# Performance work log

Measured on AMD Instinct MI355X. Metric: run time of the kernel, lower is better.

## Reference

```python
import jax, jax.numpy as jnp
import numpy as np

B, S, E, Q, A = 32, 2048, 1024, 1024, 512

def setup_inputs() -> dict:
    key = jax.random.key(0)
    k1, k2, k3, k4, k5 = jax.random.split(key, 5)
    scale = lambda d: 1.0 / np.sqrt(d)
    return {
        "inputs": jax.random.normal(k1, (B, S, E), dtype=jnp.float32),
        "query": jax.random.normal(k2, (B, Q), dtype=jnp.float32),
        "W_in": jax.random.normal(k3, (E, A), dtype=jnp.float32) * scale(E),
        "W_q": jax.random.normal(k4, (Q, A), dtype=jnp.float32) * scale(Q),
        "w_att": jax.random.normal(k5, (A,), dtype=jnp.float32) * scale(A),
    }

def reference(inputs, query, W_in, W_q, w_att):
    # projected inputs: [B, S, A]
    proj_in = jnp.einsum("bse,ea->bsa", inputs, W_in)
    # projected query, broadcast over S: [B, 1, A]
    proj_q = (query @ W_q)[:, None, :]
    # additive scores: [B, S]
    scores = jnp.einsum("bsa,a->bs", jnp.tanh(proj_in + proj_q), w_att)
    weights = jax.nn.softmax(scores, axis=1)  # over sequence dim
    # context over PROJECTED inputs (as in original): [B, A]
    context = jnp.einsum("bs,bsa->ba", weights, proj_in)
    return context
```

## Files before the change

### kernel.cpp

```cpp
#include <hip/hip_runtime.h>
#include <hip/hip_fp16.h>
#include <cstdint>
#include <cstddef>

#define Bb 32
#define Ss 2048
#define Ee 1024
#define Qq 1024
#define Aa 512

typedef _Float16 half8 __attribute__((ext_vector_type(8)));
typedef _Float16 half4 __attribute__((ext_vector_type(4)));
typedef float f32x4 __attribute__((ext_vector_type(4)));

#define WS_PROJQ 0u
#define WS_MPART 65536u
#define WS_LPART 69632u
#define WS_CTXP  73728u
#define WS_WWS   2170880u

__device__ __forceinline__ float fast_tanh(float x) {
  float e = __expf(2.0f * x);
  return 1.0f - __fdividef(2.0f, e + 1.0f);
}

__global__ void k_convw(const float* __restrict__ win, _Float16* __restrict__ wws) {
  int gid = blockIdx.x * 256 + threadIdx.x;
  int a  = gid & 511;
  int ks = (gid >> 9) & 3;
  int kt = gid >> 11;
  int k0 = kt * 32 + ks * 8;
  half8 v;
  #pragma unroll
  for (int j = 0; j < 8; ++j) v[j] = (_Float16)win[(size_t)(k0 + j) * Aa + a];
  *(half8*)(wws + ((size_t)kt * 16384 + (size_t)ks * 4096 + (size_t)a * 8)) = v;
}

__global__ void k_projq(const float* __restrict__ query, const float* __restrict__ wq,
                        float* __restrict__ projq) {
  __shared__ float red[256];
  int b  = blockIdx.y;
  int al = threadIdx.x & 63;
  int eq = threadIdx.x >> 6;
  int a  = blockIdx.x * 64 + al;
  const float* q = query + (size_t)b * Qq;
  float s = 0.f;
  int e0 = eq * 256;
  #pragma unroll 4
  for (int e = e0; e < e0 + 256; ++e)
    s += q[e] * wq[(size_t)e * Aa + a];
  red[threadIdx.x] = s;
  __syncthreads();
  if (eq == 0)
    projq[(size_t)b * Aa + a] = red[al] + red[al + 64] + red[al + 128] + red[al + 192];
}

__global__ __launch_bounds__(512, 4)
void k_main(const float* __restrict__ inp, const _Float16* __restrict__ wws,
            const float* __restrict__ projq, const float* __restrict__ watt,
            float* __restrict__ mpart, float* __restrict__ lpart,
            float* __restrict__ ctxp)
{
  __shared__ __align__(16) char pool[73728];
  _Float16* AldsB = (_Float16*)pool;
  _Float16* BldsB = (_Float16*)(pool + 8192);

  const int tid = threadIdx.x;
  const int l   = tid & 63;
  const int w   = tid >> 6;
  const int lr  = l & 15;
  const int kb  = l >> 4;
  const int wr  = w >> 2;
  const int wc  = w & 3;
  const int b   = blockIdx.y;
  const int ch  = blockIdx.x;

  const int arow = tid >> 3;
  const int kq   = tid & 7;
  const float* asrc = inp + ((size_t)(b * Ss + ch * 64 + arow)) * Ee + kq * 4;
  const int awoff = ((kq >> 1) * 64 + arow) * 8 + (kq & 1) * 4;

  const char* bsrc0 = (const char*)wws + (size_t)tid * 16;

  f32x4 acc[2][8];
  #pragma unroll
  for (int m = 0; m < 2; ++m)
    #pragma unroll
    for (int n = 0; n < 8; ++n) acc[m][n] = (f32x4){0.f, 0.f, 0.f, 0.f};

  {
    float4 x = *(const float4*)(asrc);
    half4 h; h[0]=(_Float16)x.x; h[1]=(_Float16)x.y; h[2]=(_Float16)x.z; h[3]=(_Float16)x.w;
    *(half4*)(AldsB + awoff) = h;
    #pragma unroll
    for (int i = 0; i < 4; ++i)
      __builtin_amdgcn_global_load_lds(
        (const __attribute__((address_space(1))) void*)(bsrc0 + i * 8192),
        (__attribute__((address_space(3))) void*)(pool + 8192 + tid * 16 + i * 8192),
        16, 0, 0);
  }
  float4 areg = *(const float4*)(asrc + 32);
  __syncthreads();

  int p = 0;
  for (int kt = 0; kt < 32; ++kt) {
    if (kt < 31) {
      half4 h; h[0]=(_Float16)areg.x; h[1]=(_Float16)areg.y; h[2]=(_Float16)areg.z; h[3]=(_Float16)areg.w;
      *(half4*)(AldsB + (p ^ 1) * 2048 + awoff) = h;
      const char* bs = bsrc0 + (size_t)(kt + 1) * 32768;
      #pragma unroll
      for (int i = 0; i < 4; ++i)
        __builtin_amdgcn_global_load_lds(
          (const __attribute__((address_space(1))) void*)(bs + i * 8192),
          (__attribute__((address_space(3))) void*)(pool + 8192 + (p ^ 1) * 32768 + tid * 16 + i * 8192),
          16, 0, 0);
    }
    __builtin_amdgcn_sched_barrier(0);
    const int ktn2 = (kt < 30) ? kt + 2 : 31;
    float4 anext = *(const float4*)(asrc + (size_t)ktn2 * 32);
    __builtin_amdgcn_sched_barrier(0);

    const _Float16* Ap = AldsB + p * 2048;
    half8 af0 = *(const half8*)(Ap + (kb * 64 + wr * 32 +      lr) * 8);
    half8 af1 = *(const half8*)(Ap + (kb * 64 + wr * 32 + 16 + lr) * 8);
    const _Float16* Bp = BldsB + p * 16384 + (kb * 512 + wc * 128 + lr) * 8;
    half8 bf0 = *(const half8*)(Bp);
    half8 bf1 = *(const half8*)(Bp + 16 * 8);
    half8 bf2 = *(const half8*)(Bp + 32 * 8);
    half8 bf3 = *(const half8*)(Bp + 48 * 8);

    acc[0][0] = __builtin_amdgcn_mfma_f32_16x16x32_f16(af0, bf0, acc[0][0], 0, 0, 0);
    acc[1][0] = __builtin_amdgcn_mfma_f32_16x16x32_f16(af1, bf0, acc[1][0], 0, 0, 0);
    acc[0][1] = __builtin_amdgcn_mfma_f32_16x16x32_f16(af0, bf1, acc[0][1], 0, 0, 0);
    acc[1][1] = __builtin_amdgcn_mfma_f32_16x16x32_f16(af1, bf1, acc[1][1], 0, 0, 0);
    acc[0][2] = __builtin_amdgcn_mfma_f32_16x16x32_f16(af0, bf2, acc[0][2], 0, 0, 0);
    acc[1][2] = __builtin_amdgcn_mfma_f32_16x16x32_f16(af1, bf2, acc[1][2], 0, 0, 0);
    acc[0][3] = __builtin_amdgcn_mfma_f32_16x16x32_f16(af0, bf3, acc[0][3], 0, 0, 0);
    acc[1][3] = __builtin_amdgcn_mfma_f32_16x16x32_f16(af1, bf3, acc[1][3], 0, 0, 0);

    half8 bf4 = *(const half8*)(Bp + 64 * 8);
    half8 bf5 = *(const half8*)(Bp + 80 * 8);
    half8 bf6 = *(const half8*)(Bp + 96 * 8);
    half8 bf7 = *(const half8*)(Bp + 112 * 8);
    acc[0][4] = __builtin_amdgcn_mfma_f32_16x16x32_f16(af0, bf4, acc[0][4], 0, 0, 0);
    acc[1][4] = __builtin_amdgcn_mfma_f32_16x16x32_f16(af1, bf4, acc[1][4], 0, 0, 0);
    acc[0][5] = __builtin_amdgcn_mfma_f32_16x16x32_f16(af0, bf5, acc[0][5], 0, 0, 0);
    acc[1][5] = __builtin_amdgcn_mfma_f32_16x16x32_f16(af1, bf5, acc[1][5], 0, 0, 0);
    acc[0][6] = __builtin_amdgcn_mfma_f32_16x16x32_f16(af0, bf6, acc[0][6], 0, 0, 0);
    acc[1][6] = __builtin_amdgcn_mfma_f32_16x16x32_f16(af1, bf6, acc[1][6], 0, 0, 0);
    acc[0][7] = __builtin_amdgcn_mfma_f32_16x16x32_f16(af0, bf7, acc[0][7], 0, 0, 0);
    acc[1][7] = __builtin_amdgcn_mfma_f32_16x16x32_f16(af1, bf7, acc[1][7], 0, 0, 0);

    __builtin_amdgcn_sched_barrier(0);
    asm volatile("s_waitcnt vmcnt(1)" ::: "memory");
    asm volatile("s_waitcnt lgkmcnt(0)" ::: "memory");
    __builtin_amdgcn_sched_barrier(0);
    __builtin_amdgcn_s_barrier();
    __builtin_amdgcn_sched_barrier(0);

    p ^= 1;
    areg = anext;
  }

  __syncthreads();
  float* pq_s = (float*)pool;
  float* wa_s = (float*)(pool + 2048);
  float (*sc4)[4] = (float(*)[4])(pool + 4096);
  float* pbuf = (float*)(pool + 5120);
  float (*ctx2)[512] = (float(*)[512])(pool + 8192);

  pq_s[tid] = projq[(size_t)b * Aa + tid];
  wa_s[tid] = watt[tid];
  __syncthreads();

  float sp[2][4];
  #pragma unroll
  for (int m = 0; m < 2; ++m)
    #pragma unroll
    for (int j = 0; j < 4; ++j) sp[m][j] = 0.f;

  #pragma unroll
  for (int n = 0; n < 8; ++n) {
    int col = wc * 128 + n * 16 + lr;
    float wan = wa_s[col], pqn = pq_s[col];
    #pragma unroll
    for (int m = 0; m < 2; ++m)
      #pragma unroll
      for (int j = 0; j < 4; ++j)
        sp[m][j] += fast_tanh(acc[m][n][j] + pqn) * wan;
  }
  #pragma unroll
  for (int m = 0; m < 2; ++m)
    #pragma unroll
    for (int j = 0; j < 4; ++j) {
      float v = sp[m][j];
      v += __shfl_xor(v, 1);
      v += __shfl_xor(v, 2);
      v += __shfl_xor(v, 4);
      v += __shfl_xor(v, 8);
      sp[m][j] = v;
    }
  if (lr == 0) {
    #pragma unroll
    for (int m = 0; m < 2; ++m)
      #pragma unroll
      for (int j = 0; j < 4; ++j)
        sc4[wr * 32 + m * 16 + kb * 4 + j][wc] = sp[m][j];
  }
  __syncthreads();

  const int pi = b * 32 + ch;
  if (tid < 64) {
    float s = sc4[tid][0] + sc4[tid][1] + sc4[tid][2] + sc4[tid][3];
    float mx = s;
    #pragma unroll
    for (int off = 1; off < 64; off <<= 1) mx = fmaxf(mx, __shfl_xor(mx, off));
    float pe = __expf(s - mx);
    float ls = pe;
    #pragma unroll
    for (int off = 1; off < 64; off <<= 1) ls += __shfl_xor(ls, off);
    pbuf[tid] = pe;
    if (tid == 0) { mpart[pi] = mx; lpart[pi] = ls; }
  }
  __syncthreads();

  float cv[8];
  #pragma unroll
  for (int n = 0; n < 8; ++n) cv[n] = 0.f;
  #pragma unroll
  for (int m = 0; m < 2; ++m)
    #pragma unroll
    for (int j = 0; j < 4; ++j) {
      float pw = pbuf[wr * 32 + m * 16 + kb * 4 + j];
      #pragma unroll
      for (int n = 0; n < 8; ++n) cv[n] += pw * acc[m][n][j];
    }
  #pragma unroll
  for (int n = 0; n < 8; ++n) {
    float v = cv[n];
    v += __shfl_xor(v, 16);
    v += __shfl_xor(v, 32);
    cv[n] = v;
  }
  if (l < 16) {
    #pragma unroll
    for (int n = 0; n < 8; ++n) ctx2[wr][wc * 128 + n * 16 + l] = cv[n];
  }
  __syncthreads();

  ctxp[(size_t)pi * 512 + tid] = ctx2[0][tid] + ctx2[1][tid];
}

__global__ void k_comb(const float* __restrict__ mpart, const float* __restrict__ lpart,
                       const float* __restrict__ ctxp, float* __restrict__ out) {
  int b = blockIdx.x, a = threadIdx.x;
  float Mg = -1e30f;
  #pragma unroll 8
  for (int i = 0; i < 32; ++i) Mg = fmaxf(Mg, mpart[b * 32 + i]);
  float den = 0.f, s = 0.f;
  #pragma unroll 8
  for (int i = 0; i < 32; ++i) {
    float e = __expf(mpart[b * 32 + i] - Mg);
    den += lpart[b * 32 + i] * e;
    s   += ctxp[((size_t)(b * 32 + i)) * 512 + a] * e;
  }
  out[(size_t)b * 512 + a] = s / den;
}

extern "C" void kernel_launch(void* const* d_in, const int* in_sizes, int n_in,
                              void* d_out, int out_size, void* d_ws, size_t ws_size,
                              hipStream_t stream) {
  const float* inputs = (const float*)d_in[0];
  const float* query  = (const float*)d_in[1];
  const float* W_in   = (const float*)d_in[2];
  const float* W_q    = (const float*)d_in[3];
  const float* w_att  = (const float*)d_in[4];
  float* out = (float*)d_out;

  char* ws = (char*)d_ws;
  float*    projq = (float*)(ws + WS_PROJQ);
  float*    mpart = (float*)(ws + WS_MPART);
  float*    lpart = (float*)(ws + WS_LPART);
  float*    ctxp  = (float*)(ws + WS_CTXP);
  _Float16* wws   = (_Float16*)(ws + WS_WWS);

  k_convw<<<256, 256, 0, stream>>>(W_in, wws);
  k_projq<<<dim3(8, 32), 256, 0, stream>>>(query, W_q, projq);
  k_main<<<dim3(32, 32), 512, 0, stream>>>(inputs, wws, projq, w_att, mpart, lpart, ctxp);
  k_comb<<<32, 512, 0, stream>>>(mpart, lpart, ctxp, out);
}
```

Baseline: 145.4 us.

## Restructure main GEMM to 64-wide K tiles with per-wave column ownership

The main fused kernel now processes K in 16 steps of 64 instead of 32 steps of 32, so it needs half as many block barriers. Each wave owns a 64-column slice across all 64 rows (a 4x4 MFMA tile), where before the waves were split 2x4 over rows and columns. The A tile is loaded as 8 halves per thread, MFMA groups are wrapped in s_setprio, and the final context is written straight to global without an LDS reduction. LDS per block doubles to 144KB and the occupancy hint drops to 2, which may limit how much latency other blocks can hide.

```diff
diff --git a/kernel.cpp b/kernel.cpp
--- a/kernel.cpp
+++ b/kernel.cpp
@@ -10,7 +10,6 @@
 #define Aa 512
 
 typedef _Float16 half8 __attribute__((ext_vector_type(8)));
-typedef _Float16 half4 __attribute__((ext_vector_type(4)));
 typedef float f32x4 __attribute__((ext_vector_type(4)));
 
 #define WS_PROJQ 0u
@@ -23,6 +22,8 @@
   float e = __expf(2.0f * x);
   return 1.0f - __fdividef(2.0f, e + 1.0f);
 }
+
+#define MFMA16(d, a8, b8) d = __builtin_amdgcn_mfma_f32_16x16x32_f16(a8, b8, d, 0, 0, 0)
 
 __global__ void k_convw(const float* __restrict__ win, _Float16* __restrict__ wws) {
   int gid = blockIdx.x * 256 + threadIdx.x;
@@ -55,142 +56,164 @@
     projq[(size_t)b * Aa + a] = red[al] + red[al + 64] + red[al + 128] + red[al + 192];
 }
 
-__global__ __launch_bounds__(512, 4)
+__global__ __launch_bounds__(512, 2)
 void k_main(const float* __restrict__ inp, const _Float16* __restrict__ wws,
             const float* __restrict__ projq, const float* __restrict__ watt,
             float* __restrict__ mpart, float* __restrict__ lpart,
             float* __restrict__ ctxp)
 {
-  __shared__ __align__(16) char pool[73728];
+  __shared__ __align__(16) char pool[147456];
   _Float16* AldsB = (_Float16*)pool;
-  _Float16* BldsB = (_Float16*)(pool + 8192);
+  _Float16* BldsB = (_Float16*)(pool + 16384);
 
   const int tid = threadIdx.x;
   const int l   = tid & 63;
   const int w   = tid >> 6;
   const int lr  = l & 15;
   const int kb  = l >> 4;
-  const int wr  = w >> 2;
-  const int wc  = w & 3;
   const int b   = blockIdx.y;
   const int ch  = blockIdx.x;
 
   const int arow = tid >> 3;
-  const int kq   = tid & 7;
-  const float* asrc = inp + ((size_t)(b * Ss + ch * 64 + arow)) * Ee + kq * 4;
-  const int awoff = ((kq >> 1) * 64 + arow) * 8 + (kq & 1) * 4;
+  const int akq  = tid & 7;
+  const float* asrc = inp + ((size_t)(b * Ss + ch * 64 + arow)) * Ee + akq * 8;
+  const int awoff = (akq * 64 + arow) * 8;
 
   const char* bsrc0 = (const char*)wws + (size_t)tid * 16;
 
-  f32x4 acc[2][8];
-  #pragma unroll
-  for (int m = 0; m < 2; ++m)
-    #pragma unroll
-    for (int n = 0; n < 8; ++n) acc[m][n] = (f32x4){0.f, 0.f, 0.f, 0.f};
+  f32x4 acc[4][4];
+  #pragma unroll
+  for (int m = 0; m < 4; ++m)
+    #pragma unroll
+    for (int n = 0; n < 4; ++n) acc[m][n] = (f32x4){0.f, 0.f, 0.f, 0.f};
 
   {
-    float4 x = *(const float4*)(asrc);
-    half4 h; h[0]=(_Float16)x.x; h[1]=(_Float16)x.y; h[2]=(_Float16)x.z; h[3]=(_Float16)x.w;
-    *(half4*)(AldsB + awoff) = h;
-    #pragma unroll
-    for (int i = 0; i < 4; ++i)
+    #pragma unroll
+    for (int i = 0; i < 8; ++i)
       __builtin_amdgcn_global_load_lds(
         (const __attribute__((address_space(1))) void*)(bsrc0 + i * 8192),
-        (__attribute__((address_space(3))) void*)(pool + 8192 + tid * 16 + i * 8192),
+        (__attribute__((address_space(3))) void*)(pool + 16384 + tid * 16 + i * 8192),
         16, 0, 0);
-  }
-  float4 areg = *(const float4*)(asrc + 32);
-  __syncthreads();
-
-  int p = 0;
-  for (int kt = 0; kt < 32; ++kt) {
-    if (kt < 31) {
-      half4 h; h[0]=(_Float16)areg.x; h[1]=(_Float16)areg.y; h[2]=(_Float16)areg.z; h[3]=(_Float16)areg.w;
-      *(half4*)(AldsB + (p ^ 1) * 2048 + awoff) = h;
-      const char* bs = bsrc0 + (size_t)(kt + 1) * 32768;
+    float4 x0 = *(const float4*)(asrc);
+    float4 x1 = *(const float4*)(asrc + 4);
+    half8 h;
+    h[0]=(_Float16)x0.x; h[1]=(_Float16)x0.y; h[2]=(_Float16)x0.z; h[3]=(_Float16)x0.w;
+    h[4]=(_Float16)x1.x; h[5]=(_Float16)x1.y; h[6]=(_Float16)x1.z; h[7]=(_Float16)x1.w;
+    *(half8*)(AldsB + awoff) = h;
+  }
+  __syncthreads();
+
+  int pp = 0;
+  for (int t = 0; t < 16; ++t) {
+    const _Float16* Abase = AldsB + pp * 4096;
+    const _Float16* Bbase = BldsB + pp * 32768;
+
+    half8 bf0 = *(const half8*)(Bbase + (kb * 512 + w * 64      + lr) * 8);
+    half8 bf1 = *(const half8*)(Bbase + (kb * 512 + w * 64 + 16 + lr) * 8);
+    half8 bf2 = *(const half8*)(Bbase + (kb * 512 + w * 64 + 32 + lr) * 8);
+    half8 bf3 = *(const half8*)(Bbase + (kb * 512 + w * 64 + 48 + lr) * 8);
+    half8 af0 = *(const half8*)(Abase + (kb * 64      + lr) * 8);
+    half8 af1 = *(const half8*)(Abase + (kb * 64 + 16 + lr) * 8);
+
+    float4 aL0, aL1;
+    if (t < 15) {
+      const char* bs = bsrc0 + (size_t)(t + 1) * 65536;
       #pragma unroll
-      for (int i = 0; i < 4; ++i)
+      for (int i = 0; i < 8; ++i)
         __builtin_amdgcn_global_load_lds(
           (const __attribute__((address_space(1))) void*)(bs + i * 8192),
-          (__attribute__((address_space(3))) void*)(pool + 8192 + (p ^ 1) * 32768 + tid * 16 + i * 8192),
+          (__attribute__((address_space(3))) void*)(pool + 16384 + (pp ^ 1) * 65536 + tid * 16 + i * 8192),
           16, 0, 0);
-    }
-    __builtin_amdgcn_sched_barrier(0);
-    const int ktn2 = (kt < 30) ? kt + 2 : 31;
-    float4 anext = *(const float4*)(asrc + (size_t)ktn2 * 32);
-    __builtin_amdgcn_sched_barrier(0);
-
-    const _Float16* Ap = AldsB + p * 2048;
-    half8 af0 = *(const half8*)(Ap + (kb * 64 + wr * 32 +      lr) * 8);
-    half8 af1 = *(const half8*)(Ap + (kb * 64 + wr * 32 + 16 + lr) * 8);
-    const _Float16* Bp = BldsB + p * 16384 + (kb * 512 + wc * 128 + lr) * 8;
-    half8 bf0 = *(const half8*)(Bp);
-    half8 bf1 = *(const half8*)(Bp + 16 * 8);
-    half8 bf2 = *(const half8*)(Bp + 32 * 8);
-    half8 bf3 = *(const half8*)(Bp + 48 * 8);
-
-    acc[0][0] = __builtin_amdgcn_mfma_f32_16x16x32_f16(af0, bf0, acc[0][0], 0, 0, 0);
-    acc[1][0] = __builtin_amdgcn_mfma_f32_16x16x32_f16(af1, bf0, acc[1][0], 0, 0, 0);
-    acc[0][1] = __builtin_amdgcn_mfma_f32_16x16x32_f16(af0, bf1, acc[0][1], 0, 0, 0);
-    acc[1][1] = __builtin_amdgcn_mfma_f32_16x16x32_f16(af1, bf1, acc[1][1], 0, 0, 0);
-    acc[0][2] = __builtin_amdgcn_mfma_f32_16x16x32_f16(af0, bf2, acc[0][2], 0, 0, 0);
-    acc[1][2] = __builtin_amdgcn_mfma_f32_16x16x32_f16(af1, bf2, acc[1][2], 0, 0, 0);
-    acc[0][3] = __builtin_amdgcn_mfma_f32_16x16x32_f16(af0, bf3, acc[0][3], 0, 0, 0);
-    acc[1][3] = __builtin_amdgcn_mfma_f32_16x16x32_f16(af1, bf3, acc[1][3], 0, 0, 0);
-
-    half8 bf4 = *(const half8*)(Bp + 64 * 8);
-    half8 bf5 = *(const half8*)(Bp + 80 * 8);
-    half8 bf6 = *(const half8*)(Bp + 96 * 8);
-    half8 bf7 = *(const half8*)(Bp + 112 * 8);
-    acc[0][4] = __builtin_amdgcn_mfma_f32_16x16x32_f16(af0, bf4, acc[0][4], 0, 0, 0);
-    acc[1][4] = __builtin_amdgcn_mfma_f32_16x16x32_f16(af1, bf4, acc[1][4], 0, 0, 0);
-    acc[0][5] = __builtin_amdgcn_mfma_f32_16x16x32_f16(af0, bf5, acc[0][5], 0, 0, 0);
-    acc[1][5] = __builtin_amdgcn_mfma_f32_16x16x32_f16(af1, bf5, acc[1][5], 0, 0, 0);
-    acc[0][6] = __builtin_amdgcn_mfma_f32_16x16x32_f16(af0, bf6, acc[0][6], 0, 0, 0);
-    acc[1][6] = __builtin_amdgcn_mfma_f32_16x16x32_f16(af1, bf6, acc[1][6], 0, 0, 0);
-    acc[0][7] = __builtin_amdgcn_mfma_f32_16x16x32_f16(af0, bf7, acc[0][7], 0, 0, 0);
-    acc[1][7] = __builtin_amdgcn_mfma_f32_16x16x32_f16(af1, bf7, acc[1][7], 0, 0, 0);
-
-    __builtin_amdgcn_sched_barrier(0);
-    asm volatile("s_waitcnt vmcnt(1)" ::: "memory");
-    asm volatile("s_waitcnt lgkmcnt(0)" ::: "memory");
-    __builtin_amdgcn_sched_barrier(0);
-    __builtin_amdgcn_s_barrier();
-    __builtin_amdgcn_sched_barrier(0);
-
-    p ^= 1;
-    areg = anext;
+      __builtin_amdgcn_sched_barrier(0);
+      const float* ap = asrc + (size_t)(t + 1) * 64;
+      aL0 = *(const float4*)(ap);
+      aL1 = *(const float4*)(ap + 4);
+      __builtin_amdgcn_sched_barrier(0);
+    }
+
+    __builtin_amdgcn_s_setprio(1);
+    MFMA16(acc[0][0], af0, bf0); MFMA16(acc[0][1], af0, bf1);
+    MFMA16(acc[0][2], af0, bf2); MFMA16(acc[0][3], af0, bf3);
+    MFMA16(acc[1][0], af1, bf0); MFMA16(acc[1][1], af1, bf1);
+    MFMA16(acc[1][2], af1, bf2); MFMA16(acc[1][3], af1, bf3);
+    __builtin_amdgcn_s_setprio(0);
+
+    half8 af2 = *(const half8*)(Abase + (kb * 64 + 32 + lr) * 8);
+    half8 af3 = *(const half8*)(Abase + (kb * 64 + 48 + lr) * 8);
+    __builtin_amdgcn_s_setprio(1);
+    MFMA16(acc[2][0], af2, bf0); MFMA16(acc[2][1], af2, bf1);
+    MFMA16(acc[2][2], af2, bf2); MFMA16(acc[2][3], af2, bf3);
+    MFMA16(acc[3][0], af3, bf0); MFMA16(acc[3][1], af3, bf1);
+    MFMA16(acc[3][2], af3, bf2); MFMA16(acc[3][3], af3, bf3);
+    __builtin_amdgcn_s_setprio(0);
+
+    bf0 = *(const half8*)(Bbase + ((4 + kb) * 512 + w * 64      + lr) * 8);
+    bf1 = *(const half8*)(Bbase + ((4 + kb) * 512 + w * 64 + 16 + lr) * 8);
+    bf2 = *(const half8*)(Bbase + ((4 + kb) * 512 + w * 64 + 32 + lr) * 8);
+    bf3 = *(const half8*)(Bbase + ((4 + kb) * 512 + w * 64 + 48 + lr) * 8);
+    af0 = *(const half8*)(Abase + ((4 + kb) * 64      + lr) * 8);
+    af1 = *(const half8*)(Abase + ((4 + kb) * 64 + 16 + lr) * 8);
+    __builtin_amdgcn_s_setprio(1);
+    MFMA16(acc[0][0], af0, bf0); MFMA16(acc[0][1], af0, bf1);
+    MFMA16(acc[0][2], af0, bf2); MFMA16(acc[0][3], af0, bf3);
+    MFMA16(acc[1][0], af1, bf0); MFMA16(acc[1][1], af1, bf1);
+    MFMA16(acc[1][2], af1, bf2); MFMA16(acc[1][3], af1, bf3);
+    __builtin_amdgcn_s_setprio(0);
+
+    af2 = *(const half8*)(Abase + ((4 + kb) * 64 + 32 + lr) * 8);
+    af3 = *(const half8*)(Abase + ((4 + kb) * 64 + 48 + lr) * 8);
+    if (t < 15) {
+      __builtin_amdgcn_sched_barrier(0);
+      half8 h;
+      h[0]=(_Float16)aL0.x; h[1]=(_Float16)aL0.y; h[2]=(_Float16)aL0.z; h[3]=(_Float16)aL0.w;
+      h[4]=(_Float16)aL1.x; h[5]=(_Float16)aL1.y; h[6]=(_Float16)aL1.z; h[7]=(_Float16)aL1.w;
+      *(half8*)(AldsB + (pp ^ 1) * 4096 + awoff) = h;
+      __builtin_amdgcn_sched_barrier(0);
+    }
+    __builtin_amdgcn_s_setprio(1);
+    MFMA16(acc[2][0], af2, bf0); MFMA16(acc[2][1], af2, bf1);
+    MFMA16(acc[2][2], af2, bf2); MFMA16(acc[2][3], af2, bf3);
+    MFMA16(acc[3][0], af3, bf0); MFMA16(acc[3][1], af3, bf1);
+    MFMA16(acc[3][2], af3, bf2); MFMA16(acc[3][3], af3, bf3);
+    __builtin_amdgcn_s_setprio(0);
+
+    if (t < 15) {
+      asm volatile("s_waitcnt lgkmcnt(0)" ::: "memory");
+      __builtin_amdgcn_sched_barrier(0);
+      __builtin_amdgcn_s_barrier();
+      __builtin_amdgcn_sched_barrier(0);
+    }
+    pp ^= 1;
   }
 
   __syncthreads();
   float* pq_s = (float*)pool;
   float* wa_s = (float*)(pool + 2048);
-  float (*sc4)[4] = (float(*)[4])(pool + 4096);
-  float* pbuf = (float*)(pool + 5120);
-  float (*ctx2)[512] = (float(*)[512])(pool + 8192);
+  float (*sc8)[8] = (float(*)[8])(pool + 4096);
+  float* pbuf = (float*)(pool + 6144);
 
   pq_s[tid] = projq[(size_t)b * Aa + tid];
   wa_s[tid] = watt[tid];
   __syncthreads();
 
-  float sp[2][4];
-  #pragma unroll
-  for (int m = 0; m < 2; ++m)
+  float sp[4][4];
+  #pragma unroll
+  for (int m = 0; m < 4; ++m)
     #pragma unroll
     for (int j = 0; j < 4; ++j) sp[m][j] = 0.f;
 
   #pragma unroll
-  for (int n = 0; n < 8; ++n) {
-    int col = wc * 128 + n * 16 + lr;
+  for (int n = 0; n < 4; ++n) {
+    int col = w * 64 + n * 16 + lr;
     float wan = wa_s[col], pqn = pq_s[col];
     #pragma unroll
-    for (int m = 0; m < 2; ++m)
+    for (int m = 0; m < 4; ++m)
       #pragma unroll
       for (int j = 0; j < 4; ++j)
         sp[m][j] += fast_tanh(acc[m][n][j] + pqn) * wan;
   }
   #pragma unroll
-  for (int m = 0; m < 2; ++m)
+  for (int m = 0; m < 4; ++m)
     #pragma unroll
     for (int j = 0; j < 4; ++j) {
       float v = sp[m][j];
@@ -202,16 +225,18 @@
     }
   if (lr == 0) {
     #pragma unroll
-    for (int m = 0; m < 2; ++m)
+    for (int m = 0; m < 4; ++m)
       #pragma unroll
       for (int j = 0; j < 4; ++j)
-        sc4[wr * 32 + m * 16 + kb * 4 + j][wc] = sp[m][j];
+        sc8[m * 16 + kb * 4 + j][w] = sp[m][j];
   }
   __syncthreads();
 
   const int pi = b * 32 + ch;
   if (tid < 64) {
-    float s = sc4[tid][0] + sc4[tid][1] + sc4[tid][2] + sc4[tid][3];
+    float s = 0.f;
+    #pragma unroll
+    for (int q = 0; q < 8; ++q) s += sc8[tid][q];
     float mx = s;
     #pragma unroll
     for (int off = 1; off < 64; off <<= 1) mx = fmaxf(mx, __shfl_xor(mx, off));
@@ -224,19 +249,19 @@
   }
   __syncthreads();
 
-  float cv[8];
-  #pragma unroll
-  for (int n = 0; n < 8; ++n) cv[n] = 0.f;
-  #pragma unroll
-  for (int m = 0; m < 2; ++m)
+  float cv[4];
+  #pragma unroll
+  for (int n = 0; n < 4; ++n) cv[n] = 0.f;
+  #pragma unroll
+  for (int m = 0; m < 4; ++m)
     #pragma unroll
     for (int j = 0; j < 4; ++j) {
-      float pw = pbuf[wr * 32 + m * 16 + kb * 4 + j];
+      float pw = pbuf[m * 16 + kb * 4 + j];
       #pragma unroll
-      for (int n = 0; n < 8; ++n) cv[n] += pw * acc[m][n][j];
-    }
-  #pragma unroll
-  for (int n = 0; n < 8; ++n) {
+      for (int n = 0; n < 4; ++n) cv[n] += pw * acc[m][n][j];
+    }
+  #pragma unroll
+  for (int n = 0; n < 4; ++n) {
     float v = cv[n];
     v += __shfl_xor(v, 16);
     v += __shfl_xor(v, 32);
@@ -244,11 +269,9 @@
   }
   if (l < 16) {
     #pragma unroll
-    for (int n = 0; n < 8; ++n) ctx2[wr][wc * 128 + n * 16 + l] = cv[n];
-  }
-  __syncthreads();
-
-  ctxp[(size_t)pi * 512 + tid] = ctx2[0][tid] + ctx2[1][tid];
+    for (int n = 0; n < 4; ++n)
+      ctxp[(size_t)pi * 512 + w * 64 + n * 16 + l] = cv[n];
+  }
 }
 
 __global__ void k_comb(const float* __restrict__ mpart, const float* __restrict__ lpart,
```

Result: slower. 175.8 us (+20.9%).

## Switch main GEMM to 32x32x16 MFMA with 1x8 wave tiling

Applied to the files above, without the earlier changes.

The projection GEMM moves from 16x16x32 MFMA tiles on a 2x4 wave grid to 32x32x16 MFMA tiles, with each wave owning all 64 rows and a 64-column slice. The aim is fewer LDS fragment reads per MFMA and larger, more efficient matrix instructions. The score and context epilogues are rewritten for the 32x32 accumulator layout, so the context is written straight from registers without an LDS reduction stage. The hand-placed waitcnt and sched barriers are replaced by a plain __syncthreads, with the A-tile LDS store moved after the MFMAs. That barrier may now also wait on the outstanding prefetch load, which could add stalls in the main loop.

```diff
diff --git a/kernel.cpp b/kernel.cpp
--- a/kernel.cpp
+++ b/kernel.cpp
@@ -11,7 +11,7 @@
 
 typedef _Float16 half8 __attribute__((ext_vector_type(8)));
 typedef _Float16 half4 __attribute__((ext_vector_type(4)));
-typedef float f32x4 __attribute__((ext_vector_type(4)));
+typedef float f32x16 __attribute__((ext_vector_type(16)));
 
 #define WS_PROJQ 0u
 #define WS_MPART 65536u
@@ -23,6 +23,8 @@
   float e = __expf(2.0f * x);
   return 1.0f - __fdividef(2.0f, e + 1.0f);
 }
+
+#define MFMA32(d, a8, b8) d = __builtin_amdgcn_mfma_f32_32x32x16_f16(a8, b8, d, 0, 0, 0)
 
 __global__ void k_convw(const float* __restrict__ win, _Float16* __restrict__ wws) {
   int gid = blockIdx.x * 256 + threadIdx.x;
@@ -68,10 +70,8 @@
   const int tid = threadIdx.x;
   const int l   = tid & 63;
   const int w   = tid >> 6;
-  const int lr  = l & 15;
-  const int kb  = l >> 4;
-  const int wr  = w >> 2;
-  const int wc  = w & 3;
+  const int lh  = l & 31;
+  const int hi  = l >> 5;
   const int b   = blockIdx.y;
   const int ch  = blockIdx.x;
 
@@ -82,11 +82,13 @@
 
   const char* bsrc0 = (const char*)wws + (size_t)tid * 16;
 
-  f32x4 acc[2][8];
+  f32x16 acc[2][2];
   #pragma unroll
   for (int m = 0; m < 2; ++m)
     #pragma unroll
-    for (int n = 0; n < 8; ++n) acc[m][n] = (f32x4){0.f, 0.f, 0.f, 0.f};
+    for (int n = 0; n < 2; ++n)
+      #pragma unroll
+      for (int r = 0; r < 16; ++r) acc[m][n][r] = 0.f;
 
   {
     float4 x = *(const float4*)(asrc);
@@ -105,8 +107,6 @@
   int p = 0;
   for (int kt = 0; kt < 32; ++kt) {
     if (kt < 31) {
-      half4 h; h[0]=(_Float16)areg.x; h[1]=(_Float16)areg.y; h[2]=(_Float16)areg.z; h[3]=(_Float16)areg.w;
-      *(half4*)(AldsB + (p ^ 1) * 2048 + awoff) = h;
       const char* bs = bsrc0 + (size_t)(kt + 1) * 32768;
       #pragma unroll
       for (int i = 0; i < 4; ++i)
@@ -115,49 +115,33 @@
           (__attribute__((address_space(3))) void*)(pool + 8192 + (p ^ 1) * 32768 + tid * 16 + i * 8192),
           16, 0, 0);
     }
-    __builtin_amdgcn_sched_barrier(0);
     const int ktn2 = (kt < 30) ? kt + 2 : 31;
     float4 anext = *(const float4*)(asrc + (size_t)ktn2 * 32);
-    __builtin_amdgcn_sched_barrier(0);
 
     const _Float16* Ap = AldsB + p * 2048;
-    half8 af0 = *(const half8*)(Ap + (kb * 64 + wr * 32 +      lr) * 8);
-    half8 af1 = *(const half8*)(Ap + (kb * 64 + wr * 32 + 16 + lr) * 8);
-    const _Float16* Bp = BldsB + p * 16384 + (kb * 512 + wc * 128 + lr) * 8;
-    half8 bf0 = *(const half8*)(Bp);
-    half8 bf1 = *(const half8*)(Bp + 16 * 8);
-    half8 bf2 = *(const half8*)(Bp + 32 * 8);
-    half8 bf3 = *(const half8*)(Bp + 48 * 8);
-
-    acc[0][0] = __builtin_amdgcn_mfma_f32_16x16x32_f16(af0, bf0, acc[0][0], 0, 0, 0);
-    acc[1][0] = __builtin_amdgcn_mfma_f32_16x16x32_f16(af1, bf0, acc[1][0], 0, 0, 0);
-    acc[0][1] = __builtin_amdgcn_mfma_f32_16x16x32_f16(af0, bf1, acc[0][1], 0, 0, 0);
-    acc[1][1] = __builtin_amdgcn_mfma_f32_16x16x32_f16(af1, bf1, acc[1][1], 0, 0, 0);
-    acc[0][2] = __builtin_amdgcn_mfma_f32_16x16x32_f16(af0, bf2, acc[0][2], 0, 0, 0);
-    acc[1][2] = __builtin_amdgcn_mfma_f32_16x16x32_f16(af1, bf2, acc[1][2], 0, 0, 0);
-    acc[0][3] = __builtin_amdgcn_mfma_f32_16x16x32_f16(af0, bf3, acc[0][3], 0, 0, 0);
-    acc[1][3] = __builtin_amdgcn_mfma_f32_16x16x32_f16(af1, bf3, acc[1][3], 0, 0, 0);
-
-    half8 bf4 = *(const half8*)(Bp + 64 * 8);
-    half8 bf5 = *(const half8*)(Bp + 80 * 8);
-    half8 bf6 = *(const half8*)(Bp + 96 * 8);
-    half8 bf7 = *(const half8*)(Bp + 112 * 8);
-    acc[0][4] = __builtin_amdgcn_mfma_f32_16x16x32_f16(af0, bf4, acc[0][4], 0, 0, 0);
-    acc[1][4] = __builtin_amdgcn_mfma_f32_16x16x32_f16(af1, bf4, acc[1][4], 0, 0, 0);
-    acc[0][5] = __builtin_amdgcn_mfma_f32_16x16x32_f16(af0, bf5, acc[0][5], 0, 0, 0);
-    acc[1][5] = __builtin_amdgcn_mfma_f32_16x16x32_f16(af1, bf5, acc[1][5], 0, 0, 0);
-    acc[0][6] = __builtin_amdgcn_mfma_f32_16x16x32_f16(af0, bf6, acc[0][6], 0, 0, 0);
-    acc[1][6] = __builtin_amdgcn_mfma_f32_16x16x32_f16(af1, bf6, acc[1][6], 0, 0, 0);
-    acc[0][7] = __builtin_amdgcn_mfma_f32_16x16x32_f16(af0, bf7, acc[0][7], 0, 0, 0);
-    acc[1][7] = __builtin_amdgcn_mfma_f32_16x16x32_f16(af1, bf7, acc[1][7], 0, 0, 0);
-
-    __builtin_amdgcn_sched_barrier(0);
-    asm volatile("s_waitcnt vmcnt(1)" ::: "memory");
-    asm volatile("s_waitcnt lgkmcnt(0)" ::: "memory");
-    __builtin_amdgcn_sched_barrier(0);
-    __builtin_amdgcn_s_barrier();
-    __builtin_amdgcn_sched_barrier(0);
-
+    const _Float16* Bp = BldsB + p * 16384;
+    {
+      half8 af0 = *(const half8*)(Ap + ((hi) * 64 +      lh) * 8);
+      half8 af1 = *(const half8*)(Ap + ((hi) * 64 + 32 + lh) * 8);
+      half8 bf0 = *(const half8*)(Bp + ((hi) * 512 + w * 64 +      lh) * 8);
+      half8 bf1 = *(const half8*)(Bp + ((hi) * 512 + w * 64 + 32 + lh) * 8);
+      MFMA32(acc[0][0], af0, bf0); MFMA32(acc[0][1], af0, bf1);
+      MFMA32(acc[1][0], af1, bf0); MFMA32(acc[1][1], af1, bf1);
+    }
+    {
+      half8 af0 = *(const half8*)(Ap + ((2 + hi) * 64 +      lh) * 8);
+      half8 af1 = *(const half8*)(Ap + ((2 + hi) * 64 + 32 + lh) * 8);
+      half8 bf0 = *(const half8*)(Bp + ((2 + hi) * 512 + w * 64 +      lh) * 8);
+      half8 bf1 = *(const half8*)(Bp + ((2 + hi) * 512 + w * 64 + 32 + lh) * 8);
+      MFMA32(acc[0][0], af0, bf0); MFMA32(acc[0][1], af0, bf1);
+      MFMA32(acc[1][0], af1, bf0); MFMA32(acc[1][1], af1, bf1);
+    }
+
+    if (kt < 31) {
+      half4 h; h[0]=(_Float16)areg.x; h[1]=(_Float16)areg.y; h[2]=(_Float16)areg.z; h[3]=(_Float16)areg.w;
+      *(half4*)(AldsB + (p ^ 1) * 2048 + awoff) = h;
+    }
+    __syncthreads();
     p ^= 1;
     areg = anext;
   }
@@ -165,53 +149,36 @@
   __syncthreads();
   float* pq_s = (float*)pool;
   float* wa_s = (float*)(pool + 2048);
-  float (*sc4)[4] = (float(*)[4])(pool + 4096);
-  float* pbuf = (float*)(pool + 5120);
-  float (*ctx2)[512] = (float(*)[512])(pool + 8192);
+  float (*sc8)[8] = (float(*)[8])(pool + 4096);
+  float* pbuf = (float*)(pool + 6144);
 
   pq_s[tid] = projq[(size_t)b * Aa + tid];
   wa_s[tid] = watt[tid];
   __syncthreads();
 
-  float sp[2][4];
+  const float pq0 = pq_s[w * 64 +      lh], wa0 = wa_s[w * 64 +      lh];
+  const float pq1 = pq_s[w * 64 + 32 + lh], wa1 = wa_s[w * 64 + 32 + lh];
+
   #pragma unroll
   for (int m = 0; m < 2; ++m)
     #pragma unroll
-    for (int j = 0; j < 4; ++j) sp[m][j] = 0.f;
-
-  #pragma unroll
-  for (int n = 0; n < 8; ++n) {
-    int col = wc * 128 + n * 16 + lr;
-    float wan = wa_s[col], pqn = pq_s[col];
-    #pragma unroll
-    for (int m = 0; m < 2; ++m)
-      #pragma unroll
-      for (int j = 0; j < 4; ++j)
-        sp[m][j] += fast_tanh(acc[m][n][j] + pqn) * wan;
-  }
-  #pragma unroll
-  for (int m = 0; m < 2; ++m)
-    #pragma unroll
-    for (int j = 0; j < 4; ++j) {
-      float v = sp[m][j];
+    for (int r = 0; r < 16; ++r) {
+      float v = fast_tanh(acc[m][0][r] + pq0) * wa0 + fast_tanh(acc[m][1][r] + pq1) * wa1;
       v += __shfl_xor(v, 1);
       v += __shfl_xor(v, 2);
       v += __shfl_xor(v, 4);
       v += __shfl_xor(v, 8);
-      sp[m][j] = v;
-    }
-  if (lr == 0) {
-    #pragma unroll
-    for (int m = 0; m < 2; ++m)
-      #pragma unroll
-      for (int j = 0; j < 4; ++j)
-        sc4[wr * 32 + m * 16 + kb * 4 + j][wc] = sp[m][j];
-  }
+      v += __shfl_xor(v, 16);
+      if (lh == 0)
+        sc8[m * 32 + (r & 3) + 8 * (r >> 2) + 4 * hi][w] = v;
+    }
   __syncthreads();
 
   const int pi = b * 32 + ch;
   if (tid < 64) {
-    float s = sc4[tid][0] + sc4[tid][1] + sc4[tid][2] + sc4[tid][3];
+    float s = 0.f;
+    #pragma unroll
+    for (int q = 0; q < 8; ++q) s += sc8[tid][q];
     float mx = s;
     #pragma unroll
     for (int off = 1; off < 64; off <<= 1) mx = fmaxf(mx, __shfl_xor(mx, off));
@@ -224,31 +191,21 @@
   }
   __syncthreads();
 
-  float cv[8];
-  #pragma unroll
-  for (int n = 0; n < 8; ++n) cv[n] = 0.f;
+  float cv0 = 0.f, cv1 = 0.f;
   #pragma unroll
   for (int m = 0; m < 2; ++m)
     #pragma unroll
-    for (int j = 0; j < 4; ++j) {
-      float pw = pbuf[wr * 32 + m * 16 + kb * 4 + j];
-      #pragma unroll
-      for (int n = 0; n < 8; ++n) cv[n] += pw * acc[m][n][j];
-    }
-  #pragma unroll
-  for (int n = 0; n < 8; ++n) {
-    float v = cv[n];
-    v += __shfl_xor(v, 16);
-    v += __shfl_xor(v, 32);
-    cv[n] = v;
-  }
-  if (l < 16) {
-    #pragma unroll
-    for (int n = 0; n < 8; ++n) ctx2[wr][wc * 128 + n * 16 + l] = cv[n];
-  }
-  __syncthreads();
-
-  ctxp[(size_t)pi * 512 + tid] = ctx2[0][tid] + ctx2[1][tid];
+    for (int r = 0; r < 16; ++r) {
+      float pw = pbuf[m * 32 + (r & 3) + 8 * (r >> 2) + 4 * hi];
+      cv0 += pw * acc[m][0][r];
+      cv1 += pw * acc[m][1][r];
+    }
+  cv0 += __shfl_xor(cv0, 32);
+  cv1 += __shfl_xor(cv1, 32);
+  if (l < 32) {
+    ctxp[(size_t)pi * 512 + w * 64 +      l] = cv0;
+    ctxp[(size_t)pi * 512 + w * 64 + 32 + l] = cv1;
+  }
 }
 
 __global__ void k_comb(const float* __restrict__ mpart, const float* __restrict__ lpart,
```

After: 158.2 us. +8.8%, slower.
